# Kernel tuning notes

Hardware: AMD Instinct MI355X
Metric: run time of the kernel (lower is better)

Reference implementation:

```python
import jax, jax.numpy as jnp
import numpy as np

SCALE = 2
K_UP = 5
K_ENC = 3


def _conv(x, w, b, pad):
    # NCHW conv, OIHW weights
    y = jax.lax.conv_general_dilated(
        x, w, window_strides=(1, 1), padding=((pad, pad), (pad, pad)),
        dimension_numbers=('NCHW', 'OIHW', 'NCHW'))
    return y + b[None, :, None, None]


def setup_inputs() -> dict:
    key = jax.random.key(0)
    k0, k1, k2 = jax.random.split(key, 3)
    b, c, h, w = 4, 256, 64, 64
    c_mid = 64
    n_kernel = SCALE * SCALE * K_UP * K_UP  # 100
    x = jax.random.normal(k0, (b, c, h, w), jnp.float32)
    w1 = jax.random.normal(k1, (c_mid, c, K_ENC, K_ENC), jnp.float32) * 0.02
    b1 = jnp.zeros((c_mid,), jnp.float32)
    w2 = jax.random.normal(k2, (n_kernel, c_mid, 1, 1), jnp.float32) * 0.02
    b2 = jnp.zeros((n_kernel,), jnp.float32)
    return {"x": x, "w1": w1, "b1": b1, "w2": w2, "b2": b2}


def reference(x, w1, b1, w2, b2):
    b, c, h, w = x.shape
    s, k = SCALE, K_UP
    # kernel prediction encoder: 3x3 conv -> ReLU -> 1x1 conv
    feat = jax.nn.relu(_conv(x, w1, b1, K_ENC // 2))
    kern = _conv(feat, w2, b2, 0)                     # (b, s^2*k^2, h, w)
    kern = jax.nn.softmax(kern, axis=1)               # softmax over full channel dim (as in source)
    kern = kern.reshape(b, s * s, k * k, h, w)
    # F.unfold(x, k, padding=k//2) -> (b, c, k^2, h, w); torch ordering: kh major, kw minor
    pad = k // 2
    xp = jnp.pad(x, ((0, 0), (0, 0), (pad, pad), (pad, pad)))
    patches = jnp.stack([xp[:, :, i:i + h, j:j + w]
                         for i in range(k) for j in range(k)], axis=2)  # (b, c, k^2, h, w)
    # per-pixel weighted reassembly: sum over k^2 neighborhood
    out = jnp.einsum('bskhw,bckhw->bschw', kern, patches)  # (b, s^2, c, h, w)
    # view(b, s^2*c, h, w) then pixel_shuffle(scale), exactly matching torch semantics
    out = out.reshape(b, s * s * c, h, w)
    cout = (s * s * c) // (s * s)
    out = out.reshape(b, cout, s, s, h, w)
    out = out.transpose(0, 1, 4, 2, 5, 3).reshape(b, cout, h * s, w * s)
    return out
```

## Files before the change

kernel.cpp:

```cpp
#include <hip/hip_runtime.h>


#define BB 4
#define CC 256
#define HH 64
#define WW 64
#define CMID 64
#define NKCH 100

typedef __bf16 bf16;
typedef __bf16 bf16x8 __attribute__((ext_vector_type(8)));
typedef float f32x4 __attribute__((ext_vector_type(4)));

#define BAR_LGKM() asm volatile("s_waitcnt lgkmcnt(0)\n\ts_barrier" ::: "memory")

__device__ __forceinline__ void async_copy16(const void* gsrc, void* ldst) {
    __builtin_amdgcn_global_load_lds(
        (__attribute__((address_space(1))) void*)(void*)gsrc,
        (__attribute__((address_space(3))) void*)ldst, 16, 0, 0);
}

__global__ void k0a_transform(const float* __restrict__ w1, const float* __restrict__ w2,
                              bf16* __restrict__ w1c, bf16* __restrict__ w2c) {
    int c8 = blockIdx.x;
    int oq = blockIdx.y;
    int tid = threadIdx.x;
    __shared__ __align__(16) float wf[16 * 300];

    for (int i = tid; i < 16 * 72; i += 256) {
        int o = i / 72, r = i % 72;
        *(float4*)&wf[o * 300 + r * 4] =
            *(const float4*)&w1[(size_t)(oq * 16 + o) * 2304 + c8 * 288 + r * 4];
    }
    __syncthreads();

    for (int t = tid; t < 576; t += 256) {
        int o = t & 15, q = (t >> 4) & 3, kk = t >> 6;
        union { bf16 h[8]; uint4 u; } v;
        #pragma unroll
        for (int i8 = 0; i8 < 8; ++i8)
            v.h[i8] = (bf16)wf[o * 300 + (q * 8 + i8) * 9 + kk];
        *(uint4*)&w1c[(size_t)((((c8 * 9 + kk) * 4 + q) * 64) + oq * 16 + o) * 8] = v.u;
    }

    if (c8 == 0 && oq == 0) {
        for (int i = tid; i < 7168; i += 256) {
            int i8 = i & 7;
            int oc = (i >> 3) % 112;
            int kq = (i >> 3) / 112;
            int ic = (kq >> 2) * 32 + (kq & 3) * 8 + i8;
            w2c[i] = (oc < NKCH) ? (bf16)w2[oc * 64 + ic] : (bf16)0.f;
        }
    }
}

__global__ __launch_bounds__(512) void k123_fused(const float* __restrict__ x,
        const bf16* __restrict__ w1c, const bf16* __restrict__ w2c,
        const float* __restrict__ b1, const float* __restrict__ b2,
        float* __restrict__ out) {
    int bh = blockIdx.x;
    int b = bh >> 6, h = bh & 63;
    int tid = threadIdx.x;
    int lane = tid & 63, wid = tid >> 6;
    int l15 = lane & 15, quad = lane >> 4;
    int mhalf = wid & 1, nq = wid >> 1;

    __shared__ __align__(16) char smem[131584];
    bf16*  xs0  = (bf16*)smem;
    bf16*  xs1  = (bf16*)(smem + 12800);
    bf16*  wl0  = (bf16*)(smem + 25600);
    bf16*  wl1  = (bf16*)(smem + 62464);
    bf16*  fsb  = (bf16*)(smem + 99328);
    float* ls   = (float*)(smem + 25600);
    float* kts  = (float*)(smem + 62464);
    float* red  = (float*)smem;

    const float* xb = x + (size_t)b * (CC * HH * WW);

    int g0 = wid & 3, r0 = wid >> 2;
    bool tv1 = (wid < 4);
    int hr0 = h - 1 + r0;
    int hr1 = h + 1;
    bool vm0 = (hr0 >= 0 && hr0 < HH);
    bool vm1 = (hr1 < HH);

    float fA[16], fB[16];
    #define LOADX(C8, F)                                                          \
        {                                                                         \
            if (vm0) {                                                            \
                const float* s0 = xb + ((size_t)((C8) * 32 + g0 * 8) * (HH * WW)) \
                                 + hr0 * WW + lane;                               \
                _Pragma("unroll")                                                 \
                for (int i = 0; i < 8; ++i) F[i] = s0[(size_t)i * (HH * WW)];     \
            }                                                                     \
            if (tv1 && vm1) {                                                     \
                const float* s1 = xb + ((size_t)((C8) * 32 + g0 * 8) * (HH * WW)) \
                                 + hr1 * WW + lane;                               \
                _Pragma("unroll")                                                 \
                for (int i = 0; i < 8; ++i) F[8 + i] = s1[(size_t)i * (HH * WW)]; \
            }                                                                     \
        }
    #define WRITEB(F, XSDST)                                                      \
        {                                                                         \
            if (vm0) {                                                            \
                union { bf16 hh[8]; uint4 u; } cv;                                \
                _Pragma("unroll")                                                 \
                for (int i = 0; i < 8; ++i) cv.hh[i] = (bf16)F[i];                \
                *(uint4*)&(XSDST)[((r0 * 4 + g0) * 66 + 1 + lane) * 8] = cv.u;    \
            }                                                                     \
            if (tv1 && vm1) {                                                     \
                union { bf16 hh[8]; uint4 u; } cv;                                \
                _Pragma("unroll")                                                 \
                for (int i = 0; i < 8; ++i) cv.hh[i] = (bf16)F[8 + i];            \
                *(uint4*)&(XSDST)[((2 * 4 + g0) * 66 + 1 + lane) * 8] = cv.u;     \
            }                                                                     \
        }
    #define ACOPY(C8, WDST)                                                       \
        for (int t = wid; t < 36; t += 8)                                         \
            async_copy16(w1c + ((((C8) * 36 + t) << 9) + lane * 8), (void*)&(WDST)[t << 9]);
    #define MFMAS(XSRC, WSRC)                                                     \
        _Pragma("unroll")                                                         \
        for (int kk = 0; kk < 9; ++kk) {                                          \
            int r3 = kk / 3, kw = kk % 3;                                         \
            bf16x8 a0 = *(const bf16x8*)&(WSRC)[((kk * 4 + quad) * 64 + mhalf * 32 + l15) * 8]; \
            bf16x8 a1 = *(const bf16x8*)&(WSRC)[((kk * 4 + quad) * 64 + mhalf * 32 + 16 + l15) * 8]; \
            bf16x8 xv = *(const bf16x8*)&(XSRC)[((r3 * 4 + quad) * 66 + nq * 16 + l15 + kw) * 8]; \
            acc0 = __builtin_amdgcn_mfma_f32_16x16x32_bf16(a0, xv, acc0, 0, 0, 0); \
            acc1 = __builtin_amdgcn_mfma_f32_16x16x32_bf16(a1, xv, acc1, 0, 0, 0); \
        }

    for (int i = tid; i < 6336; i += 512) { xs0[i] = (bf16)0.f; xs1[i] = (bf16)0.f; }
    LOADX(0, fA)
    ACOPY(0, wl0)
    __syncthreads();
    WRITEB(fA, xs0)
    LOADX(1, fB)
    __syncthreads();

    f32x4 acc0 = {0.f, 0.f, 0.f, 0.f}, acc1 = {0.f, 0.f, 0.f, 0.f};

    for (int c8 = 0; c8 < 8; c8 += 2) {
        ACOPY(c8 + 1, wl1)
        if (c8 < 6) { LOADX(c8 + 2, fA) }
        MFMAS(xs0, wl0)
        WRITEB(fB, xs1)
        __syncthreads();
        if (c8 < 6) { ACOPY(c8 + 2, wl0) }
        if (c8 < 6) { LOADX(c8 + 3, fB) }
        MFMAS(xs1, wl1)
        if (c8 < 6) { WRITEB(fA, xs0) }
        __syncthreads();
    }

    int px = nq * 16 + l15;
    #pragma unroll
    for (int mi = 0; mi < 2; ++mi) {
        int oc0 = mhalf * 32 + mi * 16 + quad * 4;
        float4 bv = *(const float4*)&b1[oc0];
        f32x4 v = mi ? acc1 : acc0;
        union { bf16 hh[4]; unsigned long long u; } o;
        o.hh[0] = (bf16)fmaxf(v[0] + bv.x, 0.f);
        o.hh[1] = (bf16)fmaxf(v[1] + bv.y, 0.f);
        o.hh[2] = (bf16)fmaxf(v[2] + bv.z, 0.f);
        o.hh[3] = (bf16)fmaxf(v[3] + bv.w, 0.f);
        *(unsigned long long*)&fsb[px * 72 + oc0] = o.u;
    }
    __syncthreads();

    int t8 = tid & 255, h2 = tid >> 8;
    int w3 = t8 & 63, cg3 = t8 >> 6;
    #define XLOAD(P, V)                                                          \
        _Pragma("unroll")                                                        \
        for (int k = 0; k < 5; ++k) {                                            \
            int idx = t8 + k * 256;                                              \
            int u = idx & 15, cc = (idx >> 4) & 15, rr = idx >> 8;               \
            int hr = h - 2 + rr;                                                 \
            V[k] = make_float4(0.f, 0.f, 0.f, 0.f);                              \
            if (hr >= 0 && hr < HH)                                              \
                V[k] = *(const float4*)&x[(((size_t)b * CC + (2 * (P) + h2) * 16 + cc) * HH + hr) * WW + 4 * u]; \
        }
    #define XWRITE(V, TB)                                                        \
        _Pragma("unroll")                                                        \
        for (int k = 0; k < 5; ++k) {                                            \
            int idx = t8 + k * 256;                                              \
            int u = idx & 15, cc = (idx >> 4) & 15, rr = idx >> 8;               \
            int bse = (rr * 4 + (cc >> 2)) * 68;                                 \
            int c = cc & 3;                                                      \
            _Pragma("unroll")                                                    \
            for (int j = 0; j < 4; ++j) {                                        \
                int s = 2 + 4 * u + j;                                           \
                int sw = s ^ ((s >> 3) & 7);                                     \
                (TB)[(bse + sw) * 4 + c] = ((const float*)&V[k])[j];             \
            }                                                                    \
        }
    float4 xst[5];
    XLOAD(0, xst)

    if (wid < 7) {
        f32x4 lacc0 = {0.f,0.f,0.f,0.f}, lacc1 = {0.f,0.f,0.f,0.f};
        f32x4 lacc2 = {0.f,0.f,0.f,0.f}, lacc3 = {0.f,0.f,0.f,0.f};
        #pragma unroll
        for (int kk = 0; kk < 2; ++kk) {
            bf16x8 a = *(const bf16x8*)&w2c[(((kk * 4 + quad) * 112) + wid * 16 + l15) * 8];
            bf16x8 bf0 = *(const bf16x8*)&fsb[( 0 + l15) * 72 + kk * 32 + quad * 8];
            bf16x8 bf1 = *(const bf16x8*)&fsb[(16 + l15) * 72 + kk * 32 + quad * 8];
            bf16x8 bf2 = *(const bf16x8*)&fsb[(32 + l15) * 72 + kk * 32 + quad * 8];
            bf16x8 bf3 = *(const bf16x8*)&fsb[(48 + l15) * 72 + kk * 32 + quad * 8];
            lacc0 = __builtin_amdgcn_mfma_f32_16x16x32_bf16(a, bf0, lacc0, 0, 0, 0);
            lacc1 = __builtin_amdgcn_mfma_f32_16x16x32_bf16(a, bf1, lacc1, 0, 0, 0);
            lacc2 = __builtin_amdgcn_mfma_f32_16x16x32_bf16(a, bf2, lacc2, 0, 0, 0);
            lacc3 = __builtin_amdgcn_mfma_f32_16x16x32_bf16(a, bf3, lacc3, 0, 0, 0);
        }
        f32x4 laccs[4] = {lacc0, lacc1, lacc2, lacc3};
        #pragma unroll
        for (int nt = 0; nt < 4; ++nt)
            #pragma unroll
            for (int j = 0; j < 4; ++j) {
                int oc = wid * 16 + quad * 4 + j;
                if (oc < NKCH) ls[oc * 64 + nt * 16 + l15] = laccs[nt][j];
            }
    }
    BAR_LGKM();

    int w = lane;
    int g = wid, s2 = g & 3, ihalf = g >> 2;
    int i0 = ihalf ? 13 : 0;

    float lg[13];
    #pragma unroll
    for (int ii = 0; ii < 13; ++ii) {
        int idx = i0 + ii;
        bool act = (idx < 25);
        int oc = s2 * 25 + (act ? idx : 0);
        lg[ii] = act ? (ls[oc * 64 + w] + b2[oc]) : -1e30f;
    }

    float m = -1e30f;
    #pragma unroll
    for (int ii = 0; ii < 13; ++ii) m = fmaxf(m, lg[ii]);
    red[g * 64 + w] = m;
    BAR_LGKM();
    m = fmaxf(fmaxf(fmaxf(red[0 * 64 + w], red[1 * 64 + w]),
                    fmaxf(red[2 * 64 + w], red[3 * 64 + w])),
              fmaxf(fmaxf(red[4 * 64 + w], red[5 * 64 + w]),
                    fmaxf(red[6 * 64 + w], red[7 * 64 + w])));
    float ssum = 0.f;
    #pragma unroll
    for (int ii = 0; ii < 13; ++ii) { lg[ii] = __expf(lg[ii] - m); ssum += lg[ii]; }
    red[512 + g * 64 + w] = ssum;
    BAR_LGKM();
    ssum = ((red[512 + 0 * 64 + w] + red[512 + 1 * 64 + w]) +
            (red[512 + 2 * 64 + w] + red[512 + 3 * 64 + w])) +
           ((red[512 + 4 * 64 + w] + red[512 + 5 * 64 + w]) +
            (red[512 + 6 * 64 + w] + red[512 + 7 * 64 + w]));
    float inv = 1.f / ssum;
    #pragma unroll
    for (int ii = 0; ii < 13; ++ii)
        if (i0 + ii < 25) kts[((i0 + ii) * 64 + w) * 4 + s2] = lg[ii] * inv;
    BAR_LGKM();

    #pragma unroll
    for (int reg = 0; reg < 4; ++reg) {
        const int tb = (reg == 0) ? 0 : (reg == 1) ? 21760 : (reg == 2) ? 88064 : 109824;
        if (tid < 320) {
            int c = tid & 3, q = (tid >> 2) & 3, rg = tid >> 4;
            int slot = (q < 2) ? q : (q + 64);
            ((float*)(smem + tb))[(rg * 68 + slot) * 4 + c] = 0.f;
        }
    }

    float* tb0 = (float*)(smem + (h2 ? 21760 : 0));
    float* tb1 = (float*)(smem + (h2 ? 109824 : 88064));

    int swk[5];
    #pragma unroll
    for (int kw = 0; kw < 5; ++kw) {
        int s = w3 + kw;
        swk[kw] = s ^ ((s >> 3) & 7);
    }

    XWRITE(xst, tb0)
    BAR_LGKM();

    for (int p = 0; p < 8; ++p) {
        if (p < 7) { XLOAD(p + 1, xst) }
        float* T = (p & 1) ? tb1 : tb0;
        f32x4 a0 = {0.f,0.f,0.f,0.f}, a1 = {0.f,0.f,0.f,0.f};
        f32x4 a2 = {0.f,0.f,0.f,0.f}, a3 = {0.f,0.f,0.f,0.f};
        #pragma unroll
        for (int r = 0; r < 5; ++r) {
            #pragma unroll
            for (int kw = 0; kw < 5; ++kw) {
                f32x4 kvv = *(const f32x4*)&kts[((r * 5 + kw) * 64 + w3) * 4];
                f32x4 xv = *(const f32x4*)&T[((r * 4 + cg3) * 68 + swk[kw]) * 4];
                a0 += kvv.x * xv;
                a1 += kvv.y * xv;
                a2 += kvv.z * xv;
                a3 += kvv.w * xv;
            }
        }
        int cq = (2 * p + h2) * 4 + cg3;
        f32x4 accs[4] = {a0, a1, a2, a3};
        #pragma unroll
        for (int s = 0; s < 4; ++s) {
            size_t base = (((size_t)b * 256 + s * 64 + cq) * 128 + 2 * h) * 128 + 2 * w3;
            *(float2*)&out[base]       = make_float2(accs[s][0], accs[s][1]);
            *(float2*)&out[base + 128] = make_float2(accs[s][2], accs[s][3]);
        }
        if (p < 7) {
            float* Tnext = (p & 1) ? tb0 : tb1;
            XWRITE(xst, Tnext)
        }
        BAR_LGKM();
    }
    #undef LOADX
    #undef WRITEB
    #undef ACOPY
    #undef MFMAS
    #undef XLOAD
    #undef XWRITE
}

extern "C" void kernel_launch(void* const* d_in, const int* in_sizes, int n_in,
                              void* d_out, int out_size, void* d_ws, size_t ws_size,
                              hipStream_t stream) {
    const float* x  = (const float*)d_in[0];
    const float* w1 = (const float*)d_in[1];
    const float* b1 = (const float*)d_in[2];
    const float* w2 = (const float*)d_in[3];
    const float* b2 = (const float*)d_in[4];
    float* out = (float*)d_out;

    char* wsb = (char*)d_ws;
    bf16* w1c = (bf16*)wsb;
    bf16* w2c = (bf16*)(wsb + 294912);

    k0a_transform<<<dim3(8, 4), 256, 0, stream>>>(w1, w2, w1c, w2c);
    k123_fused<<<dim3(BB * HH), 512, 0, stream>>>(x, w1c, w2c, b1, b2, out);
}
```

Baseline: 121.9 us.

## Read conv weights directly from global instead of staging through LDS

Drops the async global-to-LDS double-buffered copy of the bf16 3x3 conv weights and has each wave load its MFMA A-operands straight from global memory (L2/L1-cached). This shrinks the shared memory footprint and removes the LDS write traffic for weights, and the smem regions for the later stages are re-laid out to match. Barriers become waitcnt lgkm + s_barrier. The cost is more global load latency inside the MFMA loop with no explicit prefetch, since every block rereads the weights from cache.

```diff
diff --git a/kernel.cpp b/kernel.cpp
--- a/kernel.cpp
+++ b/kernel.cpp
@@ -13,12 +13,6 @@
 typedef float f32x4 __attribute__((ext_vector_type(4)));
 
 #define BAR_LGKM() asm volatile("s_waitcnt lgkmcnt(0)\n\ts_barrier" ::: "memory")
-
-__device__ __forceinline__ void async_copy16(const void* gsrc, void* ldst) {
-    __builtin_amdgcn_global_load_lds(
-        (__attribute__((address_space(1))) void*)(void*)gsrc,
-        (__attribute__((address_space(3))) void*)ldst, 16, 0, 0);
-}
 
 __global__ void k0a_transform(const float* __restrict__ w1, const float* __restrict__ w2,
                               bf16* __restrict__ w1c, bf16* __restrict__ w2c) {
@@ -65,15 +59,13 @@
     int l15 = lane & 15, quad = lane >> 4;
     int mhalf = wid & 1, nq = wid >> 1;
 
-    __shared__ __align__(16) char smem[131584];
+    __shared__ __align__(16) char smem[115968];
     bf16*  xs0  = (bf16*)smem;
     bf16*  xs1  = (bf16*)(smem + 12800);
-    bf16*  wl0  = (bf16*)(smem + 25600);
-    bf16*  wl1  = (bf16*)(smem + 62464);
-    bf16*  fsb  = (bf16*)(smem + 99328);
-    float* ls   = (float*)(smem + 25600);
-    float* kts  = (float*)(smem + 62464);
-    float* red  = (float*)smem;
+    bf16*  fsb  = (bf16*)(smem + 25600);
+    float* ls   = (float*)(smem + 34816);
+    float* red  = (float*)(smem + 60416);
+    float* kts  = (float*)(smem + 68608);
 
     const float* xb = x + (size_t)b * (CC * HH * WW);
 
@@ -115,15 +107,14 @@
                 *(uint4*)&(XSDST)[((2 * 4 + g0) * 66 + 1 + lane) * 8] = cv.u;     \
             }                                                                     \
         }
-    #define ACOPY(C8, WDST)                                                       \
-        for (int t = wid; t < 36; t += 8)                                         \
-            async_copy16(w1c + ((((C8) * 36 + t) << 9) + lane * 8), (void*)&(WDST)[t << 9]);
-    #define MFMAS(XSRC, WSRC)                                                     \
+    #define MFMAS(XSRC, C8)                                                       \
         _Pragma("unroll")                                                         \
         for (int kk = 0; kk < 9; ++kk) {                                          \
             int r3 = kk / 3, kw = kk % 3;                                         \
-            bf16x8 a0 = *(const bf16x8*)&(WSRC)[((kk * 4 + quad) * 64 + mhalf * 32 + l15) * 8]; \
-            bf16x8 a1 = *(const bf16x8*)&(WSRC)[((kk * 4 + quad) * 64 + mhalf * 32 + 16 + l15) * 8]; \
+            const bf16* wp = w1c + ((size_t)((((C8) * 9 + kk) * 4 + quad) * 64    \
+                                             + mhalf * 32 + l15) * 8);            \
+            bf16x8 a0 = *(const bf16x8*)wp;                                       \
+            bf16x8 a1 = *(const bf16x8*)(wp + 128);                               \
             bf16x8 xv = *(const bf16x8*)&(XSRC)[((r3 * 4 + quad) * 66 + nq * 16 + l15 + kw) * 8]; \
             acc0 = __builtin_amdgcn_mfma_f32_16x16x32_bf16(a0, xv, acc0, 0, 0, 0); \
             acc1 = __builtin_amdgcn_mfma_f32_16x16x32_bf16(a1, xv, acc1, 0, 0, 0); \
@@ -131,25 +122,22 @@
 
     for (int i = tid; i < 6336; i += 512) { xs0[i] = (bf16)0.f; xs1[i] = (bf16)0.f; }
     LOADX(0, fA)
-    ACOPY(0, wl0)
-    __syncthreads();
+    BAR_LGKM();
     WRITEB(fA, xs0)
     LOADX(1, fB)
-    __syncthreads();
+    BAR_LGKM();
 
     f32x4 acc0 = {0.f, 0.f, 0.f, 0.f}, acc1 = {0.f, 0.f, 0.f, 0.f};
 
     for (int c8 = 0; c8 < 8; c8 += 2) {
-        ACOPY(c8 + 1, wl1)
         if (c8 < 6) { LOADX(c8 + 2, fA) }
-        MFMAS(xs0, wl0)
+        MFMAS(xs0, c8)
         WRITEB(fB, xs1)
-        __syncthreads();
-        if (c8 < 6) { ACOPY(c8 + 2, wl0) }
+        BAR_LGKM();
         if (c8 < 6) { LOADX(c8 + 3, fB) }
-        MFMAS(xs1, wl1)
+        MFMAS(xs1, c8 + 1)
         if (c8 < 6) { WRITEB(fA, xs0) }
-        __syncthreads();
+        BAR_LGKM();
     }
 
     int px = nq * 16 + l15;
@@ -165,7 +153,7 @@
         o.hh[3] = (bf16)fmaxf(v[3] + bv.w, 0.f);
         *(unsigned long long*)&fsb[px * 72 + oc0] = o.u;
     }
-    __syncthreads();
+    BAR_LGKM();
 
     int t8 = tid & 255, h2 = tid >> 8;
     int w3 = t8 & 63, cg3 = t8 >> 6;
@@ -261,7 +249,7 @@
 
     #pragma unroll
     for (int reg = 0; reg < 4; ++reg) {
-        const int tb = (reg == 0) ? 0 : (reg == 1) ? 21760 : (reg == 2) ? 88064 : 109824;
+        const int tb = (reg == 0) ? 0 : (reg == 1) ? 21760 : (reg == 2) ? 43520 : 94208;
         if (tid < 320) {
             int c = tid & 3, q = (tid >> 2) & 3, rg = tid >> 4;
             int slot = (q < 2) ? q : (q + 64);
@@ -270,7 +258,7 @@
     }
 
     float* tb0 = (float*)(smem + (h2 ? 21760 : 0));
-    float* tb1 = (float*)(smem + (h2 ? 109824 : 88064));
+    float* tb1 = (float*)(smem + (h2 ? 94208 : 43520));
 
     int swk[5];
     #pragma unroll
@@ -315,7 +303,6 @@
     }
     #undef LOADX
     #undef WRITEB
-    #undef ACOPY
     #undef MFMAS
     #undef XLOAD
     #undef XWRITE
```

New measurement: 128.3 us. 5.2% more time.
